# Performance work log

Measured on AMD Instinct MI355X. Metric: run time of the kernel, lower is better.

The kernel has to match this reference:

```python
import jax, jax.numpy as jnp
import numpy as np

INPUT_SIZE = 512
HIDDEN_SIZE = 1024
SEQ_LEN = 512
BATCH = 64


def _xavier(key, shape):
    fan_out, fan_in = shape
    limit = float(np.sqrt(6.0 / (fan_in + fan_out)))
    return jax.random.uniform(key, shape, jnp.float32, -limit, limit)


def setup_inputs() -> dict:
    key = jax.random.key(0)
    ks = jax.random.split(key, 10)
    return {
        "x_seq": jax.random.normal(ks[0], (SEQ_LEN, BATCH, INPUT_SIZE), jnp.float32),
        "h": jax.random.normal(ks[1], (BATCH, HIDDEN_SIZE), jnp.float32),
        "U_c": _xavier(ks[2], (HIDDEN_SIZE, INPUT_SIZE)),
        "w_c": jax.random.normal(ks[3], (HIDDEN_SIZE,), jnp.float32),
        "b_c": jax.random.normal(ks[4], (HIDDEN_SIZE,), jnp.float32),
        "U_a": _xavier(ks[5], (HIDDEN_SIZE, INPUT_SIZE)),
        "w_a": jax.random.normal(ks[6], (HIDDEN_SIZE,), jnp.float32),
        "b_a": jax.random.normal(ks[7], (HIDDEN_SIZE,), jnp.float32),
        "U_h": _xavier(ks[8], (HIDDEN_SIZE, INPUT_SIZE)),
        "b_h": jax.random.normal(ks[9], (HIDDEN_SIZE,), jnp.float32),
    }


def reference(x_seq, h, U_c, w_c, b_c, U_a, w_a, b_a, U_h, b_h):
    # Precompute all input projections in one big batched GEMM each:
    # (S, B, I) @ (I, H) -> (S, B, H)
    xc = jnp.einsum("sbi,hi->sbh", x_seq, U_c) + b_c
    xa = jnp.einsum("sbi,hi->sbh", x_seq, U_a) + b_a
    xh = jnp.einsum("sbi,hi->sbh", x_seq, U_h) + b_h

    def step(h, proj):
        pc, pa, ph = proj
        c = jax.nn.sigmoid(pc + w_c * h)
        a = 1.0 + jnp.tanh(pa + w_a * h)
        h_new = c * h + (1.0 - c) * jnp.tanh(ph + a * h)
        return h_new, h_new

    hn, y_seq = jax.lax.scan(step, h, (xc, xa, xh))
    return y_seq, hn
```

## Files before the change

### kernel.cpp

```cpp
#include <hip/hip_runtime.h>
#include <hip/hip_bf16.h>
#include <stdint.h>

#define SEQLEN 512
#define NBATCH 64
#define KDIM   512
#define HDIM   1024
#define MTOT   (SEQLEN * NBATCH)
#define NTOT   (3 * HDIM)
#define STRIDE (NBATCH * HDIM)

typedef __attribute__((ext_vector_type(4))) float f32x4;
typedef _Float16 f16x8 __attribute__((ext_vector_type(8)));

__global__ __launch_bounds__(256) void cvt_x(const float* __restrict__ x,
                                             _Float16* __restrict__ xh,
                                             _Float16* __restrict__ xl) {
    int i = blockIdx.x * 256 + threadIdx.x;
    const float4* s = (const float4*)(x + (size_t)i * 8);
    float4 a = s[0], b = s[1];
    float v[8] = {a.x, a.y, a.z, a.w, b.x, b.y, b.z, b.w};
    f16x8 hi, lo;
#pragma unroll
    for (int j = 0; j < 8; ++j) {
        _Float16 h = (_Float16)v[j];
        hi[j] = h;
        lo[j] = (_Float16)(v[j] - (float)h);
    }
    *(f16x8*)(xh + (size_t)i * 8) = hi;
    *(f16x8*)(xl + (size_t)i * 8) = lo;
}

__global__ __launch_bounds__(256) void cvt_u(const float* __restrict__ Uc,
                                             const float* __restrict__ Ua,
                                             const float* __restrict__ Uh,
                                             _Float16* __restrict__ uh,
                                             _Float16* __restrict__ ul) {
    int i = blockIdx.x * 256 + threadIdx.x;
    int n = i >> 6;
    int kb = (i & 63) * 8;
    const float* src = (n < HDIM) ? (Uc + (size_t)n * KDIM)
                     : (n < 2 * HDIM) ? (Ua + (size_t)(n - HDIM) * KDIM)
                     : (Uh + (size_t)(n - 2 * HDIM) * KDIM);
    const float4* s = (const float4*)(src + kb);
    float4 a = s[0], b = s[1];
    float v[8] = {a.x, a.y, a.z, a.w, b.x, b.y, b.z, b.w};
    f16x8 hi, lo;
#pragma unroll
    for (int j = 0; j < 8; ++j) {
        _Float16 h = (_Float16)v[j];
        hi[j] = h;
        lo[j] = (_Float16)(v[j] - (float)h);
    }
    *(f16x8*)(uh + (size_t)n * KDIM + kb) = hi;
    *(f16x8*)(ul + (size_t)n * KDIM + kb) = lo;
}

#define BM 256
#define BN 128
#define BK 32
#define NT_N (NTOT / BN)
#define GRID ((MTOT / BM) * NT_N)
#define KT_N (KDIM / BK)
#define OFF_AH 0
#define OFF_AL 8192
#define OFF_BH 16384
#define OFF_BL 20480
#define BUF_HW 24576

__device__ __forceinline__ void gload16(const _Float16* g, _Float16* l) {
    __builtin_amdgcn_global_load_lds((const __attribute__((address_space(1))) void*)g,
                                     (__attribute__((address_space(3))) void*)l,
                                     16, 0, 0);
}

__device__ __forceinline__ f32x4 mfma16(f16x8 a, f16x8 b, f32x4 c) {
    return __builtin_amdgcn_mfma_f32_16x16x32_f16(a, b, c, 0, 0, 0);
}

__global__ __launch_bounds__(512, 2) void gemm_f16x2(const _Float16* __restrict__ Ah,
                                                     const _Float16* __restrict__ Al,
                                                     const _Float16* __restrict__ Bh,
                                                     const _Float16* __restrict__ Bl,
                                                     float* __restrict__ pc,
                                                     float* __restrict__ pa,
                                                     float* __restrict__ ph) {
    __shared__ _Float16 lds[3][BUF_HW];

    int bid  = blockIdx.x;
    int bm   = bid / NT_N;
    int bn   = bid % NT_N;
    int tid  = threadIdx.x;
    int lane = tid & 63;
    int wave = tid >> 6;
    int wr   = wave >> 1;
    int wc   = wave & 1;

    size_t row_off = (size_t)(tid >> 2) * KDIM
                   + (size_t)(((tid & 3) ^ ((tid >> 3) & 3)) * 8);
    const _Float16* gAh = Ah + (size_t)bm * BM * KDIM + row_off;
    const _Float16* gAl = Al + (size_t)bm * BM * KDIM + row_off;
    const _Float16* gBh = Bh + (size_t)bn * BN * KDIM + row_off;
    const _Float16* gBl = Bl + (size_t)bn * BN * KDIM + row_off;
    const size_t P128 = (size_t)128 * KDIM;
    int t8 = tid * 8;

#define STAGE(buf, kt) do { int _g = (kt) * BK;                                \
    gload16(gAh + _g,        &lds[buf][OFF_AH + t8]);                          \
    gload16(gAh + P128 + _g, &lds[buf][OFF_AH + 4096 + t8]);                   \
    gload16(gAl + _g,        &lds[buf][OFF_AL + t8]);                          \
    gload16(gAl + P128 + _g, &lds[buf][OFF_AL + 4096 + t8]);                   \
    gload16(gBh + _g,        &lds[buf][OFF_BH + t8]);                          \
    gload16(gBl + _g,        &lds[buf][OFF_BL + t8]); } while (0)

    f32x4 acc[4][4];
#pragma unroll
    for (int i = 0; i < 4; ++i)
#pragma unroll
        for (int j = 0; j < 4; ++j)
            acc[i][j] = (f32x4){0.f, 0.f, 0.f, 0.f};

    int ro = lane & 15;
    int ko = ((lane >> 4) ^ ((lane >> 1) & 3)) * 8;

    f16x8 a_[4][2], b_[4][2];

#define READ_A(cb) _Pragma("unroll")                                           \
    for (int i = 0; i < 4; ++i) {                                              \
        int row = wr * 64 + i * 16 + ro;                                       \
        a_[i][0] = *(const f16x8*)(&lds[cb][OFF_AH + row * BK + ko]);          \
        a_[i][1] = *(const f16x8*)(&lds[cb][OFF_AL + row * BK + ko]);          \
    }
#define READ_B(cb) _Pragma("unroll")                                           \
    for (int j = 0; j < 4; ++j) {                                              \
        int row = wc * 64 + j * 16 + ro;                                       \
        b_[j][0] = *(const f16x8*)(&lds[cb][OFF_BH + row * BK + ko]);          \
        b_[j][1] = *(const f16x8*)(&lds[cb][OFF_BL + row * BK + ko]);          \
    }
#define MFMA_ALL() _Pragma("unroll")                                           \
    for (int i = 0; i < 4; ++i) _Pragma("unroll")                              \
        for (int j = 0; j < 4; ++j) {                                          \
            f32x4 c = acc[i][j];                                               \
            c = mfma16(a_[i][0], b_[j][1], c);                      \
            c = mfma16(a_[i][1], b_[j][0], c);                      \
            c = mfma16(a_[i][0], b_[j][0], c);                      \
            acc[i][j] = c;                                                     \
        }

    STAGE(0, 0);
    STAGE(1, 1);

    int c0 = 0, c1 = 1, c2 = 2;
    for (int kt = 0; kt < KT_N; ++kt) {
        __builtin_amdgcn_sched_barrier(0);
        if (kt < KT_N - 1) asm volatile("s_waitcnt vmcnt(6)" ::: "memory");
        else               asm volatile("s_waitcnt vmcnt(0)" ::: "memory");
        __builtin_amdgcn_s_barrier();
        __builtin_amdgcn_sched_barrier(0);

        READ_B(c0);
        READ_A(c0);
        if (kt + 2 < KT_N) STAGE(c2, kt + 2);
        __builtin_amdgcn_s_setprio(1);
        MFMA_ALL();
        __builtin_amdgcn_s_setprio(0);

        int t = c0; c0 = c1; c1 = c2; c2 = t;
    }

    int n0 = bn * BN;
    float* outp = (n0 < HDIM) ? pc : (n0 < 2 * HDIM) ? pa : ph;
    int nb = n0 & (HDIM - 1);
#pragma unroll
    for (int i = 0; i < 4; ++i)
#pragma unroll
        for (int r = 0; r < 4; ++r) {
            int m = bm * BM + wr * 64 + i * 16 + (lane >> 4) * 4 + r;
#pragma unroll
            for (int j = 0; j < 4; ++j) {
                int n = nb + wc * 64 + j * 16 + (lane & 15);
                outp[(size_t)m * HDIM + n] = acc[i][j][r];
            }
        }
#undef STAGE
#undef READ_A
#undef READ_B
#undef MFMA_ALL
}

__global__ __launch_bounds__(256) void recur(const float* __restrict__ pc_a,
                                             const float* __restrict__ pa_a,
                                             float* out,
                                             const float* __restrict__ h0,
                                             const float* __restrict__ wc_,
                                             const float* __restrict__ bc_,
                                             const float* __restrict__ wa_,
                                             const float* __restrict__ ba_,
                                             const float* __restrict__ bh_) {
    int idx = blockIdx.x * 256 + threadIdx.x;
    int j = idx & (HDIM - 1);
    float h  = h0[idx];
    float wc = wc_[j], bc = bc_[j];
    float wa = wa_[j], ba = ba_[j];
    float bh = bh_[j];

#define PF 16
    float pc[PF], pa[PF], ph[PF];
#pragma unroll
    for (int u = 0; u < PF; ++u) {
        pc[u] = pc_a[(size_t)u * STRIDE + idx];
        pa[u] = pa_a[(size_t)u * STRIDE + idx];
        ph[u] = out [(size_t)u * STRIDE + idx];
    }

    for (int sb = 0; sb < SEQLEN; sb += PF) {
#pragma unroll
        for (int u = 0; u < PF; ++u) {
            int s = sb + u;
            float vc = pc[u], va = pa[u], vh = ph[u];
            int sp = s + PF; sp = (sp < SEQLEN) ? sp : (SEQLEN - 1);
            pc[u] = pc_a[(size_t)sp * STRIDE + idx];
            pa[u] = pa_a[(size_t)sp * STRIDE + idx];
            ph[u] = out [(size_t)sp * STRIDE + idx];

            float zc = (vc + bc) + wc * h;
            float za = (va + ba) + wa * h;
            float c  = 1.0f / (1.0f + expf(-zc));
            float a  = 1.0f + tanhf(za);
            float ht = tanhf((vh + bh) + a * h);
            h = c * h + (1.0f - c) * ht;
            out[(size_t)s * STRIDE + idx] = h;
        }
    }
    out[(size_t)SEQLEN * STRIDE + idx] = h;
}

extern "C" void kernel_launch(void* const* d_in, const int* in_sizes, int n_in,
                              void* d_out, int out_size, void* d_ws, size_t ws_size,
                              hipStream_t stream) {
    const float* x_seq = (const float*)d_in[0];
    const float* h0    = (const float*)d_in[1];
    const float* U_c   = (const float*)d_in[2];
    const float* w_c   = (const float*)d_in[3];
    const float* b_c   = (const float*)d_in[4];
    const float* U_a   = (const float*)d_in[5];
    const float* w_a   = (const float*)d_in[6];
    const float* b_a   = (const float*)d_in[7];
    const float* U_h   = (const float*)d_in[8];
    const float* b_h   = (const float*)d_in[9];
    float* out = (float*)d_out;

    char* ws = (char*)d_ws;
    const size_t MB = 1024 * 1024;
    float*    ws_pc = (float*)ws;
    float*    ws_pa = (float*)(ws + 128 * MB);
    _Float16* x_hi  = (_Float16*)(ws + 256 * MB);
    _Float16* x_lo  = (_Float16*)(ws + 288 * MB);
    _Float16* u_hi  = (_Float16*)(ws + 320 * MB);
    _Float16* u_lo  = (_Float16*)(ws + 323 * MB);

    cvt_x<<<dim3(MTOT * KDIM / 8 / 256), dim3(256), 0, stream>>>(x_seq, x_hi, x_lo);
    cvt_u<<<dim3(NTOT * KDIM / 8 / 256), dim3(256), 0, stream>>>(U_c, U_a, U_h, u_hi, u_lo);
    gemm_f16x2<<<dim3(GRID), dim3(512), 0, stream>>>(
        x_hi, x_lo, u_hi, u_lo, ws_pc, ws_pa, out);
    recur<<<dim3(STRIDE / 256), dim3(256), 0, stream>>>(ws_pc, ws_pa, out, h0,
                                                        w_c, b_c, w_a, b_a, b_h);
}
```

Baseline: 514.7 us.

## Double-buffer MFMA fragment registers in GEMM and merge conversion kernels

The GEMM main loop is unrolled by two and ping-pongs between two register sets of A/B fragments. The next k-tile's LDS fragments are read while the MFMAs for the current tile issue, which hides LDS read latency. Because the read-ahead needs the following buffer ready, the wait becomes vmcnt(0) each iteration, which may expose global-load latency. The x and U fp32-to-fp16 split conversions are also fused into one launch to save launch overhead, and the extra fragment registers raise register pressure.

```diff
diff --git a/kernel.cpp b/kernel.cpp
--- a/kernel.cpp
+++ b/kernel.cpp
@@ -13,11 +13,35 @@
 typedef __attribute__((ext_vector_type(4))) float f32x4;
 typedef _Float16 f16x8 __attribute__((ext_vector_type(8)));
 
-__global__ __launch_bounds__(256) void cvt_x(const float* __restrict__ x,
-                                             _Float16* __restrict__ xh,
-                                             _Float16* __restrict__ xl) {
+#define XTHREADS (MTOT * KDIM / 8)
+#define UTHREADS (NTOT * KDIM / 8)
+__global__ __launch_bounds__(256) void cvt_all(const float* __restrict__ x,
+                                               const float* __restrict__ Uc,
+                                               const float* __restrict__ Ua,
+                                               const float* __restrict__ Uh,
+                                               _Float16* __restrict__ xh,
+                                               _Float16* __restrict__ xl,
+                                               _Float16* __restrict__ uh,
+                                               _Float16* __restrict__ ul) {
     int i = blockIdx.x * 256 + threadIdx.x;
-    const float4* s = (const float4*)(x + (size_t)i * 8);
+    const float* src;
+    _Float16 *dh, *dl;
+    size_t off;
+    if (i < XTHREADS) {
+        src = x + (size_t)i * 8;
+        off = (size_t)i * 8;
+        dh = xh; dl = xl;
+    } else {
+        int u = i - XTHREADS;
+        int n = u >> 6;
+        int kb = (u & 63) * 8;
+        src = ((n < HDIM) ? (Uc + (size_t)n * KDIM)
+             : (n < 2 * HDIM) ? (Ua + (size_t)(n - HDIM) * KDIM)
+             : (Uh + (size_t)(n - 2 * HDIM) * KDIM)) + kb;
+        off = (size_t)n * KDIM + kb;
+        dh = uh; dl = ul;
+    }
+    const float4* s = (const float4*)src;
     float4 a = s[0], b = s[1];
     float v[8] = {a.x, a.y, a.z, a.w, b.x, b.y, b.z, b.w};
     f16x8 hi, lo;
@@ -27,33 +51,8 @@
         hi[j] = h;
         lo[j] = (_Float16)(v[j] - (float)h);
     }
-    *(f16x8*)(xh + (size_t)i * 8) = hi;
-    *(f16x8*)(xl + (size_t)i * 8) = lo;
-}
-
-__global__ __launch_bounds__(256) void cvt_u(const float* __restrict__ Uc,
-                                             const float* __restrict__ Ua,
-                                             const float* __restrict__ Uh,
-                                             _Float16* __restrict__ uh,
-                                             _Float16* __restrict__ ul) {
-    int i = blockIdx.x * 256 + threadIdx.x;
-    int n = i >> 6;
-    int kb = (i & 63) * 8;
-    const float* src = (n < HDIM) ? (Uc + (size_t)n * KDIM)
-                     : (n < 2 * HDIM) ? (Ua + (size_t)(n - HDIM) * KDIM)
-                     : (Uh + (size_t)(n - 2 * HDIM) * KDIM);
-    const float4* s = (const float4*)(src + kb);
-    float4 a = s[0], b = s[1];
-    float v[8] = {a.x, a.y, a.z, a.w, b.x, b.y, b.z, b.w};
-    f16x8 hi, lo;
-#pragma unroll
-    for (int j = 0; j < 8; ++j) {
-        _Float16 h = (_Float16)v[j];
-        hi[j] = h;
-        lo[j] = (_Float16)(v[j] - (float)h);
-    }
-    *(f16x8*)(uh + (size_t)n * KDIM + kb) = hi;
-    *(f16x8*)(ul + (size_t)n * KDIM + kb) = lo;
+    *(f16x8*)(dh + off) = hi;
+    *(f16x8*)(dl + off) = lo;
 }
 
 #define BM 256
@@ -123,49 +122,56 @@
     int ro = lane & 15;
     int ko = ((lane >> 4) ^ ((lane >> 1) & 3)) * 8;
 
-    f16x8 a_[4][2], b_[4][2];
-
-#define READ_A(cb) _Pragma("unroll")                                           \
+    f16x8 aX[4][2], bX[4][2], aY[4][2], bY[4][2];
+
+#define READF(aS, bS, cb) do { _Pragma("unroll")                               \
     for (int i = 0; i < 4; ++i) {                                              \
         int row = wr * 64 + i * 16 + ro;                                       \
-        a_[i][0] = *(const f16x8*)(&lds[cb][OFF_AH + row * BK + ko]);          \
-        a_[i][1] = *(const f16x8*)(&lds[cb][OFF_AL + row * BK + ko]);          \
-    }
-#define READ_B(cb) _Pragma("unroll")                                           \
+        aS[i][0] = *(const f16x8*)(&lds[cb][OFF_AH + row * BK + ko]);          \
+        aS[i][1] = *(const f16x8*)(&lds[cb][OFF_AL + row * BK + ko]);          \
+    }                                                                          \
+    _Pragma("unroll")                                                          \
     for (int j = 0; j < 4; ++j) {                                              \
         int row = wc * 64 + j * 16 + ro;                                       \
-        b_[j][0] = *(const f16x8*)(&lds[cb][OFF_BH + row * BK + ko]);          \
-        b_[j][1] = *(const f16x8*)(&lds[cb][OFF_BL + row * BK + ko]);          \
-    }
-#define MFMA_ALL() _Pragma("unroll")                                           \
+        bS[j][0] = *(const f16x8*)(&lds[cb][OFF_BH + row * BK + ko]);          \
+        bS[j][1] = *(const f16x8*)(&lds[cb][OFF_BL + row * BK + ko]);          \
+    } } while (0)
+
+#define MFMAS(aS, bS) _Pragma("unroll")                                        \
     for (int i = 0; i < 4; ++i) _Pragma("unroll")                              \
         for (int j = 0; j < 4; ++j) {                                          \
             f32x4 c = acc[i][j];                                               \
-            c = mfma16(a_[i][0], b_[j][1], c);                      \
-            c = mfma16(a_[i][1], b_[j][0], c);                      \
-            c = mfma16(a_[i][0], b_[j][0], c);                      \
+            c = mfma16(aS[i][0], bS[j][1], c);                      \
+            c = mfma16(aS[i][1], bS[j][0], c);                      \
+            c = mfma16(aS[i][0], bS[j][0], c);                      \
             acc[i][j] = c;                                                     \
         }
 
+#define BODY(kt, ACUR, BCUR, ANXT, BNXT, cbn, cbt) do {                        \
+    __builtin_amdgcn_sched_barrier(0);                                         \
+    asm volatile("s_waitcnt vmcnt(0)" ::: "memory");                           \
+    __builtin_amdgcn_s_barrier();                                              \
+    __builtin_amdgcn_sched_barrier(0);                                         \
+    if ((kt) + 1 < KT_N) READF(ANXT, BNXT, cbn);                               \
+    if ((kt) + 2 < KT_N) STAGE(cbt, (kt) + 2);                                 \
+    __builtin_amdgcn_s_setprio(1);                                             \
+    MFMAS(ACUR, BCUR);                                                         \
+    __builtin_amdgcn_s_setprio(0);                                             \
+} while (0)
+
     STAGE(0, 0);
     STAGE(1, 1);
+    __builtin_amdgcn_sched_barrier(0);
+    asm volatile("s_waitcnt vmcnt(6)" ::: "memory");
+    __builtin_amdgcn_s_barrier();
+    __builtin_amdgcn_sched_barrier(0);
+    READF(aX, bX, 0);
 
     int c0 = 0, c1 = 1, c2 = 2;
-    for (int kt = 0; kt < KT_N; ++kt) {
-        __builtin_amdgcn_sched_barrier(0);
-        if (kt < KT_N - 1) asm volatile("s_waitcnt vmcnt(6)" ::: "memory");
-        else               asm volatile("s_waitcnt vmcnt(0)" ::: "memory");
-        __builtin_amdgcn_s_barrier();
-        __builtin_amdgcn_sched_barrier(0);
-
-        READ_B(c0);
-        READ_A(c0);
-        if (kt + 2 < KT_N) STAGE(c2, kt + 2);
-        __builtin_amdgcn_s_setprio(1);
-        MFMA_ALL();
-        __builtin_amdgcn_s_setprio(0);
-
-        int t = c0; c0 = c1; c1 = c2; c2 = t;
+    for (int kt = 0; kt < KT_N; kt += 2) {
+        BODY(kt,     aX, bX, aY, bY, c1, c2);
+        BODY(kt + 1, aY, bY, aX, bX, c2, c0);
+        int t = c0; c0 = c2; c2 = c1; c1 = t;
     }
 
     int n0 = bn * BN;
@@ -183,9 +189,9 @@
             }
         }
 #undef STAGE
-#undef READ_A
-#undef READ_B
-#undef MFMA_ALL
+#undef READF
+#undef MFMAS
+#undef BODY
 }
 
 __global__ __launch_bounds__(256) void recur(const float* __restrict__ pc_a,
@@ -259,8 +265,8 @@
     _Float16* u_hi  = (_Float16*)(ws + 320 * MB);
     _Float16* u_lo  = (_Float16*)(ws + 323 * MB);
 
-    cvt_x<<<dim3(MTOT * KDIM / 8 / 256), dim3(256), 0, stream>>>(x_seq, x_hi, x_lo);
-    cvt_u<<<dim3(NTOT * KDIM / 8 / 256), dim3(256), 0, stream>>>(U_c, U_a, U_h, u_hi, u_lo);
+    cvt_all<<<dim3((XTHREADS + UTHREADS) / 256), dim3(256), 0, stream>>>(
+        x_seq, U_c, U_a, U_h, x_hi, x_lo, u_hi, u_lo);
     gemm_f16x2<<<dim3(GRID), dim3(512), 0, stream>>>(
         x_hi, x_lo, u_hi, u_lo, ws_pc, ws_pa, out);
     recur<<<dim3(STRIDE / 256), dim3(256), 0, stream>>>(ws_pc, ws_pa, out, h0,
```

Result: no change. 513.5 us (-0.2%).
